# Optimization experiments

Hardware: AMD Instinct MI355X
Metric: run time of the kernel (lower is better)

The kernel has to match this reference:

```python
import jax, jax.numpy as jnp
import numpy as np

B, T, NN = 128, 128, 8          # batch, time_window, nodes per graph (hardcoded in source)
N = B * T * NN                  # 131072 flattened node rows
F_IN, C = 32, 64                # node_features, spatial_features
E = 1_048_576                   # edges (avg degree 8)
EPS = 1e-5


def _gcn(x, src, dst, W, b):
    # PyG GCNConv: h = D^{-1/2}(A+I)D^{-1/2} X W + b, self-loops added, symmetric norm
    h = x @ W                                           # [N, C]
    loop = jnp.arange(N, dtype=src.dtype)
    s = jnp.concatenate([src, loop])
    d = jnp.concatenate([dst, loop])
    deg = jax.ops.segment_sum(jnp.ones_like(s, dtype=h.dtype), d, num_segments=N)
    dinv = jax.lax.rsqrt(deg)                           # deg >= 1 due to self loops
    msg = h[s] * (dinv[s] * dinv[d])[:, None]           # gather + scale
    out = jax.ops.segment_sum(msg, d, num_segments=N)   # scatter-add
    return out + b


def _conv2d(x, w, b, pad_w):
    y = jax.lax.conv_general_dilated(
        x, w, window_strides=(1, 1), padding=[(0, 0), (pad_w, pad_w)],
        dimension_numbers=("NCHW", "OIHW", "NCHW"))
    return y + b[None, :, None, None]


def _bn_relu(x, g, beta):
    # BatchNorm2d in training mode: batch statistics, biased variance
    mu = x.mean(axis=(0, 2, 3), keepdims=True)
    var = x.var(axis=(0, 2, 3), keepdims=True)
    y = (x - mu) * jax.lax.rsqrt(var + EPS)
    return jax.nn.relu(y * g[None, :, None, None] + beta[None, :, None, None])


def _layer(x, src, dst, gw, gb, tw, tb, bg, bb, ow, ob):
    h = _gcn(x, src, dst, gw, gb)                       # [N, C]
    h = h.reshape(B, T, NN, -1).transpose(0, 3, 2, 1)   # [B, C, NN, T]
    h = _conv2d(h, tw, tb, 1)                           # (1,3) temporal conv, pad (0,1)
    h = _bn_relu(h, bg, bb)
    h = _conv2d(h, ow, ob, 0)                           # 1x1 conv (squeeze() is a no-op here)
    h = jnp.tanh(h)
    return h.reshape(-1, h.shape[1])                    # faithful to x.view(-1, x.shape[1])


def setup_inputs() -> dict:
    key = jax.random.key(0)
    ks = jax.random.split(key, 20)
    p = lambda k, shape: (jax.random.normal(k, shape, jnp.float32) * 0.05)
    inp = {
        "x": jax.random.normal(ks[0], (N, F_IN), jnp.float32),
        "edge_index": jax.random.randint(ks[1], (2, E), 0, N, jnp.int32),
        "gcn1_w": p(ks[2], (F_IN, C)), "gcn1_b": jnp.zeros((C,), jnp.float32),
        "t1_w": p(ks[3], (C, C, 1, 3)), "t1_b": jnp.zeros((C,), jnp.float32),
        "bn1_g": jnp.ones((C,), jnp.float32), "bn1_b": jnp.zeros((C,), jnp.float32),
        "o1_w": p(ks[4], (C, C, 1, 1)), "o1_b": jnp.zeros((C,), jnp.float32),
        "gcn2_w": p(ks[5], (C, C)), "gcn2_b": jnp.zeros((C,), jnp.float32),
        "t2_w": p(ks[6], (C, C, 1, 3)), "t2_b": jnp.zeros((C,), jnp.float32),
        "bn2_g": jnp.ones((C,), jnp.float32), "bn2_b": jnp.zeros((C,), jnp.float32),
        "o2_w": p(ks[7], (C, C, 1, 1)), "o2_b": jnp.zeros((C,), jnp.float32),
        "reg_w": p(ks[8], (C, 8)), "reg_b": jnp.zeros((8,), jnp.float32),
    }
    return inp


def reference(x, edge_index, gcn1_w, gcn1_b, t1_w, t1_b, bn1_g, bn1_b, o1_w, o1_b,
              gcn2_w, gcn2_b, t2_w, t2_b, bn2_g, bn2_b, o2_w, o2_b, reg_w, reg_b):
    src, dst = edge_index[0], edge_index[1]
    h = _layer(x, src, dst, gcn1_w, gcn1_b, t1_w, t1_b, bn1_g, bn1_b, o1_w, o1_b)
    h = _layer(h, src, dst, gcn2_w, gcn2_b, t2_w, t2_b, bn2_g, bn2_b, o2_w, o2_b)
    h = h @ reg_w + reg_b                                # [N, 8]
    h = h.reshape(B, T, NN, -1)
    return h.mean(axis=(1, 3))                           # [B, NN] = [128, 8]
```

## Files before the change

kernel.cpp:

```cpp
#include <hip/hip_runtime.h>
#include <stdint.h>

typedef unsigned short u16;
typedef __attribute__((ext_vector_type(8))) short bf16x8;
typedef __attribute__((ext_vector_type(4))) float f32x4;

static const int N_NODES = 131072;
static const int N_EDGES = 1048576;

__device__ __forceinline__ float u2f(u16 u){
  union{uint32_t i; float f;} w; w.i = ((uint32_t)u)<<16; return w.f;
}
__device__ __forceinline__ u16 f2u(float f){
  union{float f; uint32_t u;} v; v.f=f;
  uint32_t u=v.u;
  u += 0x7fff + ((u>>16)&1);
  return (u16)(u>>16);
}
__device__ __forceinline__ float bits2f(uint32_t b){
  union{uint32_t i; float f;} w; w.i = b; return w.f;
}
__device__ __forceinline__ float ldv(const float* p, int i){ return p[i]; }
__device__ __forceinline__ float ldv(const u16* p, int i){ return u2f(p[i]); }
__device__ __forceinline__ void stv(float* p, int i, float v){ p[i]=v; }
__device__ __forceinline__ void stv(u16* p, int i, float v){ p[i]=f2u(v); }
__device__ __forceinline__ float ldmix(const void* p, int i, int isbf){
  return isbf ? u2f(((const u16*)p)[i]) : ((const float*)p)[i];
}

__global__ __launch_bounds__(256) void k_detect(const uint32_t* __restrict__ x, int* __restrict__ flag,
                                                float* __restrict__ stats1, float* __restrict__ stats2,
                                                float* __restrict__ zacc){
  int tid = threadIdx.x;
  for (int i=tid; i<512; i+=256){ stats1[i] = 0.f; stats2[i] = 0.f; }
  for (int i=tid; i<1024; i+=256) zacc[i] = 0.f;
  if (tid == 0){
    int cnt=0;
    for (int i=0;i<256;i++){
      uint32_t e=(x[i]>>7)&0xFFu;
      if (e>=0x6Fu && e<=0x85u) cnt++;
    }
    *flag = (cnt>=128) ? 1 : 0;
  }
}

__global__ __launch_bounds__(256) void k_hist(const int* __restrict__ dst, int* __restrict__ H){
  __shared__ int h[256];
  int tid = threadIdx.x;
  h[tid] = 0;
  __syncthreads();
  int base = blockIdx.x*4096;
  #pragma unroll
  for (int i=0;i<16;i++){
    int e = base + i*256 + tid;
    atomicAdd(&h[(dst[e] & (N_NODES-1))>>9], 1);
  }
  __syncthreads();
  H[blockIdx.x*256 + tid] = h[tid];
}

__global__ __launch_bounds__(256) void k_colscan(const int* __restrict__ H, int* __restrict__ P,
                                                 int* __restrict__ bt){
  __shared__ int sc[256];
  int b = blockIdx.x, tid = threadIdx.x;
  int v = H[tid*256 + b];
  sc[tid] = v; __syncthreads();
  for (int d=1; d<256; d<<=1){
    int o = (tid>=d) ? sc[tid-d] : 0; __syncthreads();
    sc[tid] += o; __syncthreads();
  }
  P[tid*256 + b] = sc[tid] - v;
  if (tid==255) bt[b] = sc[255];
}

__global__ __launch_bounds__(256) void k_scatter2(const int* __restrict__ src, const int* __restrict__ dst,
                                                  const int* __restrict__ P, const int* __restrict__ bt,
                                                  uint32_t* __restrict__ ebuf){
  __shared__ int cu[256], sc[256];
  int tid = threadIdx.x;
  int v = bt[tid];
  sc[tid] = v; __syncthreads();
  for (int d=1; d<256; d<<=1){
    int o = (tid>=d) ? sc[tid-d] : 0; __syncthreads();
    sc[tid] += o; __syncthreads();
  }
  cu[tid] = (sc[tid] - v) + P[blockIdx.x*256 + tid];
  __syncthreads();
  int base = blockIdx.x*4096;
  #pragma unroll
  for (int i=0;i<16;i++){
    int e = base + i*256 + tid;
    int s = src[e] & (N_NODES-1);
    int d = dst[e] & (N_NODES-1);
    int pos = atomicAdd(&cu[d>>9], 1);
    ebuf[pos] = (uint32_t)s | ((uint32_t)(d & 511) << 17);
  }
}

__global__ __launch_bounds__(512) void k_bsort2(const uint32_t* __restrict__ ebuf, const int* __restrict__ bt,
                                                const void* __restrict__ x, const int* __restrict__ flag,
                                                int* __restrict__ adj, int* __restrict__ offs,
                                                int* __restrict__ deg, float* __restrict__ dinv,
                                                u16* __restrict__ Bout){
  __shared__ uint32_t ein[5120], outs[5120];
  __shared__ int hist[512], sc[512], cu[512];
  __shared__ int sct[256];
  __shared__ float dv[512];
  int b = blockIdx.x, tid = threadIdx.x;
  if (tid < 256){ sct[tid] = bt[tid]; }
  __syncthreads();
  for (int d=1; d<256; d<<=1){
    int o = (tid < 256 && tid>=d) ? sct[tid-d] : 0; __syncthreads();
    if (tid < 256) sct[tid] += o; __syncthreads();
  }
  int lo = sct[b] - bt[b], hi = sct[b];
  int cnt = hi - lo; if (cnt > 5120) cnt = 5120; if (cnt < 0) cnt = 0;
  hist[tid] = 0;
  __syncthreads();
  for (int i=tid; i<cnt; i+=512){
    uint32_t p = ebuf[lo+i];
    ein[i] = p;
    atomicAdd(&hist[(p>>17)&511], 1);
  }
  __syncthreads();
  sc[tid] = hist[tid];
  __syncthreads();
  for (int d=1; d<512; d<<=1){
    int v = (tid>=d) ? sc[tid-d] : 0;
    __syncthreads();
    sc[tid] += v;
    __syncthreads();
  }
  {
    int ex = sc[tid] - hist[tid];
    int node = b*512 + tid;
    offs[node] = lo + ex;
    deg[node]  = hist[tid];
    float rs = rsqrtf((float)hist[tid] + 1.0f);
    dinv[node] = rs;
    dv[tid] = rs;
    cu[tid] = ex;
  }
  __syncthreads();
  for (int i=tid; i<cnt; i+=512){
    uint32_t p = ein[i];
    int pos = atomicAdd(&cu[(p>>17)&511], 1);
    outs[pos] = p & 0x1FFFFu;
  }
  __syncthreads();
  for (int i=tid; i<cnt; i+=512) adj[lo+i] = (int)outs[i];
  int isbf = *flag;
  for (int u=tid; u<16384; u+=512){
    int nl = u>>5, c = u&31;
    int idx = ((b<<9) + nl)*32 + c;
    stv(Bout, idx, dv[nl]*ldmix(x, idx, isbf));
  }
}

__device__ __forceinline__ void acc16(uint4 a, float* acc){
  acc[0] += bits2f(a.x<<16); acc[1] += bits2f(a.x&0xFFFF0000u);
  acc[2] += bits2f(a.y<<16); acc[3] += bits2f(a.y&0xFFFF0000u);
  acc[4] += bits2f(a.z<<16); acc[5] += bits2f(a.z&0xFFFF0000u);
  acc[6] += bits2f(a.w<<16); acc[7] += bits2f(a.w&0xFFFF0000u);
}
template<int F>
__global__ __launch_bounds__(256) void k_aggp2(const u16* __restrict__ Xs,
                                               const int* __restrict__ adj, const int* __restrict__ offs,
                                               const int* __restrict__ deg, const float* __restrict__ dinv,
                                               u16* __restrict__ out){
  constexpr int CH  = F/8;
  constexpr int GPW = 64/CH;
  int tid = threadIdx.x;
  int wv = tid>>6, lane = tid&63;
  int g = lane / CH;
  int k = lane % CH;
  int n = blockIdx.x*(4*GPW) + wv*GPW + g;
  int o = offs[n] & (N_EDGES-1);
  int cnt = min(deg[n], 8192);
  const uint4* X4 = (const uint4*)Xs;
  uint4 sv = X4[(size_t)n*CH + k];
  float acc[8] = {0,0,0,0,0,0,0,0};
  acc16(sv, acc);
  int e = 0;
  for (; e+8 <= cnt; e += 8){
    int i0 = adj[o+e+0] & (N_NODES-1);
    int i1 = adj[o+e+1] & (N_NODES-1);
    int i2 = adj[o+e+2] & (N_NODES-1);
    int i3 = adj[o+e+3] & (N_NODES-1);
    int i4 = adj[o+e+4] & (N_NODES-1);
    int i5 = adj[o+e+5] & (N_NODES-1);
    int i6 = adj[o+e+6] & (N_NODES-1);
    int i7 = adj[o+e+7] & (N_NODES-1);
    uint4 a0 = X4[(size_t)i0*CH + k];
    uint4 a1 = X4[(size_t)i1*CH + k];
    uint4 a2 = X4[(size_t)i2*CH + k];
    uint4 a3 = X4[(size_t)i3*CH + k];
    uint4 a4 = X4[(size_t)i4*CH + k];
    uint4 a5 = X4[(size_t)i5*CH + k];
    uint4 a6 = X4[(size_t)i6*CH + k];
    uint4 a7 = X4[(size_t)i7*CH + k];
    acc16(a0, acc); acc16(a1, acc); acc16(a2, acc); acc16(a3, acc);
    acc16(a4, acc); acc16(a5, acc); acc16(a6, acc); acc16(a7, acc);
  }
  if (e+4 <= cnt){
    int i0 = adj[o+e+0] & (N_NODES-1);
    int i1 = adj[o+e+1] & (N_NODES-1);
    int i2 = adj[o+e+2] & (N_NODES-1);
    int i3 = adj[o+e+3] & (N_NODES-1);
    uint4 a0 = X4[(size_t)i0*CH + k];
    uint4 a1 = X4[(size_t)i1*CH + k];
    uint4 a2 = X4[(size_t)i2*CH + k];
    uint4 a3 = X4[(size_t)i3*CH + k];
    acc16(a0, acc); acc16(a1, acc); acc16(a2, acc); acc16(a3, acc);
    e += 4;
  }
  for (; e < cnt; e++){
    int s = adj[o+e] & (N_NODES-1);
    uint4 a = X4[(size_t)s*CH + k];
    acc16(a, acc);
  }
  float dv = dinv[n];
  uint4 r;
  r.x = (uint32_t)f2u(acc[0]*dv) | ((uint32_t)f2u(acc[1]*dv) << 16);
  r.y = (uint32_t)f2u(acc[2]*dv) | ((uint32_t)f2u(acc[3]*dv) << 16);
  r.z = (uint32_t)f2u(acc[4]*dv) | ((uint32_t)f2u(acc[5]*dv) << 16);
  r.w = (uint32_t)f2u(acc[6]*dv) | ((uint32_t)f2u(acc[7]*dv) << 16);
  ((uint4*)out)[(size_t)n*CH + k] = r;
}

__device__ __forceinline__ void wcomb_one(int Kin, const void* gW, const void* gb, const void* tw,
                                          int isbf, u16* Wtb, float* braw, int r, int co){
  if (r < 3*Kin){
    int k = r / Kin, j = r - (r/Kin)*Kin;
    float acc = 0.f;
    for (int c=0; c<64; c++)
      acc += ldmix(gW, j*64+c, isbf) * ldmix(tw, co*192 + c*3 + k, isbf);
    Wtb[co*(3*Kin) + r] = f2u(acc);
  } else {
    int k = r - 3*Kin;
    float acc = 0.f;
    for (int c=0; c<64; c++)
      acc += ldmix(gb, c, isbf) * ldmix(tw, co*192 + c*3 + k, isbf);
    braw[k*64 + co] = acc;
  }
}
__global__ __launch_bounds__(64) void k_wcombB(const void* __restrict__ g1w, const void* __restrict__ g1b,
                                               const void* __restrict__ t1w,
                                               const void* __restrict__ g2w, const void* __restrict__ g2b,
                                               const void* __restrict__ t2w,
                                               const void* __restrict__ o1w, const void* __restrict__ o2w,
                                               const int* __restrict__ flag,
                                               u16* __restrict__ Wtb1, float* __restrict__ braw1,
                                               u16* __restrict__ Wtb2, float* __restrict__ braw2,
                                               u16* __restrict__ owb1, u16* __restrict__ owb2){
  int isbf = *flag;
  int r = blockIdx.x, co = threadIdx.x;
  if (r < 99) wcomb_one(32, g1w, g1b, t1w, isbf, Wtb1, braw1, r, co);
  else if (r < 294) wcomb_one(64, g2w, g2b, t2w, isbf, Wtb2, braw2, r-99, co);
  else if (r < 358){
    int row = r - 294;
    owb1[row*64 + co] = f2u(ldmix(o1w, row*64 + co, isbf));
  } else {
    int row = r - 358;
    owb2[row*64 + co] = f2u(ldmix(o2w, row*64 + co, isbf));
  }
}

template<int Kin>
__global__ __launch_bounds__(256) void k_tconv3(const u16* __restrict__ A, const u16* __restrict__ Wtb,
                                                const float* __restrict__ braw, const void* __restrict__ tb,
                                                const int* __restrict__ flag, u16* __restrict__ out,
                                                float* __restrict__ stats){
  constexpr int K  = 3*Kin;
  constexpr int SA = Kin + 8;
  constexpr int JH = Kin/2;
  constexpr int JL = (Kin==64) ? 5 : 4;
  __shared__ alignas(16) u16 At[66*SA];
  __shared__ float ball[64], bs0[64], bs2[64];
  __shared__ float wsum[4][64], wsum2[4][64];

  int isbf = *flag;
  int bid = blockIdx.x;
  int b = bid>>4, rem = bid&15, v = rem>>1, th = rem&1;
  const int tid = threadIdx.x;

  if (tid < 64){
    float b0=braw[tid], b1=braw[64+tid], b2=braw[128+tid];
    ball[tid] = ldmix(tb, tid, isbf) + b0 + b1 + b2;
    bs0[tid] = b0; bs2[tid] = b2;
  }
  {
    uint32_t* Ad = (uint32_t*)At;
    const uint32_t* Ag = (const uint32_t*)A;
    for (int u=tid; u<66*JH; u+=256){
      int ls = u >> JL, jd = u & (JH-1);
      int t = th*64 + ls - 1;
      uint32_t pack = 0;
      if (t >= 0 && t < 128)
        pack = Ag[((((b*128+t)*8+v))*Kin >> 1) + jd];
      Ad[ls*(SA/2) + jd] = pack;
    }
  }
  __syncthreads();

  int wv_ = tid >> 6, lane = tid & 63;
  int q = lane >> 4, l16 = lane & 15;
  int ltb0 = wv_ * 16;

  f32x4 acc[4];
  #pragma unroll
  for (int nt=0; nt<4; nt++) acc[nt] = (f32x4){0.f,0.f,0.f,0.f};

  #pragma unroll
  for (int s=0; s<K/32; s++){
    int kk = (32*s)/Kin;
    int j0 = 32*s - kk*Kin;
    int col = j0 + q*8;
    bf16x8 afr = *(const bf16x8*)&At[(ltb0 + l16 + kk)*SA + col];
    bf16x8 bfr[4];
    #pragma unroll
    for (int nt=0; nt<4; nt++){
      int co = nt*16 + l16;
      bfr[nt] = *(const bf16x8*)&Wtb[co*K + 32*s + q*8];
    }
    #pragma unroll
    for (int nt=0; nt<4; nt++)
      acc[nt] = __builtin_amdgcn_mfma_f32_16x16x32_bf16(afr, bfr[nt], acc[nt], 0, 0, 0);
  }

  float ls_[4] = {0,0,0,0}, ls2_[4] = {0,0,0,0};
  #pragma unroll
  for (int r=0; r<4; r++){
    int t = th*64 + ltb0 + q*4 + r;
    int base = (((b*128+t)*8+v)) << 6;
    #pragma unroll
    for (int nt=0; nt<4; nt++){
      int co = nt*16 + l16;
      float val = acc[nt][r] + ball[co];
      if (t == 0)   val -= bs0[co];
      if (t == 127) val -= bs2[co];
      out[base + co] = f2u(val);
      ls_[nt] += val; ls2_[nt] += val*val;
    }
  }
  #pragma unroll
  for (int nt=0; nt<4; nt++){
    ls_[nt]  += __shfl_xor(ls_[nt], 16);  ls_[nt]  += __shfl_xor(ls_[nt], 32);
    ls2_[nt] += __shfl_xor(ls2_[nt], 16); ls2_[nt] += __shfl_xor(ls2_[nt], 32);
  }
  if (q == 0){
    #pragma unroll
    for (int nt=0; nt<4; nt++){
      wsum[wv_][nt*16 + l16]  = ls_[nt];
      wsum2[wv_][nt*16 + l16] = ls2_[nt];
    }
  }
  __syncthreads();
  if (tid < 64){
    float a = wsum[0][tid]+wsum[1][tid]+wsum[2][tid]+wsum[3][tid];
    float a2 = wsum2[0][tid]+wsum2[1][tid]+wsum2[2][tid]+wsum2[3][tid];
    int bank = (bid & 3) * 128;
    atomicAdd(&stats[bank + tid], a);
    atomicAdd(&stats[bank + 64 + tid], a2);
  }
}

template<bool FINAL>
__global__ __launch_bounds__(256) void k_bnfuse3(const u16* __restrict__ X, const float* __restrict__ stats,
                                                 const void* __restrict__ gam, const void* __restrict__ bet,
                                                 const u16* __restrict__ owb, const void* __restrict__ ob,
                                                 const int* __restrict__ flag, const float* __restrict__ presc,
                                                 u16* __restrict__ out16,
                                                 float* __restrict__ zacc, const void* __restrict__ rw){
  constexpr int SA = 72;
  __shared__ alignas(16) u16 Yl[64*SA];
  __shared__ float kk[64], bsh[64], obs[64];
  __shared__ float rw_s[64];
  __shared__ float wred[4];
  int isbf = *flag;
  int bid = blockIdx.x;
  int b = bid>>4, rem = bid&15, v = rem>>1, th = rem&1;
  const int tid = threadIdx.x;
  const float invM = 1.0f/131072.0f;

  if (tid < 64){
    int ci = tid;
    float s1 = stats[ci] + stats[128+ci] + stats[256+ci] + stats[384+ci];
    float s2 = stats[64+ci] + stats[192+ci] + stats[320+ci] + stats[448+ci];
    float mu = s1*invM;
    float var = s2*invM - mu*mu;
    float rs = rsqrtf(fmaxf(var, 0.f) + 1e-5f);
    float kv = rs*ldmix(gam, ci, isbf);
    kk[ci] = kv;
    bsh[ci] = ldmix(bet, ci, isbf) - mu*kv;
    obs[ci] = ldmix(ob, ci, isbf);
    if (FINAL){
      float s = 0.f;
      #pragma unroll
      for (int f=0; f<8; f++) s += ldmix(rw, ci*8 + f, isbf);
      rw_s[ci] = s;
    }
  }
  __syncthreads();
  {
    uint32_t* Yd = (uint32_t*)Yl;
    const uint32_t* Xg = (const uint32_t*)X;
    for (int u=tid; u<64*32; u+=256){
      int lt = u>>5, jd = u&31;
      int ci = jd<<1;
      int t = th*64 + lt;
      int rowbase = (((b*128+t)*8+v)) << 6;
      uint32_t pr = Xg[(rowbase>>1) + jd];
      float x0 = bits2f(pr<<16);
      float x1 = bits2f(pr & 0xFFFF0000u);
      float y0 = fmaxf(x0*kk[ci] + bsh[ci], 0.f);
      float y1 = fmaxf(x1*kk[ci+1] + bsh[ci+1], 0.f);
      Yd[lt*(SA/2) + jd] = (uint32_t)f2u(y0) | ((uint32_t)f2u(y1) << 16);
    }
  }
  __syncthreads();

  int wv_ = tid >> 6, lane = tid & 63;
  int q = lane >> 4, l16 = lane & 15;
  int ltb0 = wv_ * 16;

  f32x4 acc[4];
  #pragma unroll
  for (int nt=0; nt<4; nt++) acc[nt] = (f32x4){0.f,0.f,0.f,0.f};

  #pragma unroll
  for (int s=0; s<2; s++){
    int col = 32*s + q*8;
    bf16x8 afr = *(const bf16x8*)&Yl[(ltb0 + l16)*SA + col];
    bf16x8 bfr[4];
    #pragma unroll
    for (int nt=0; nt<4; nt++){
      int co = nt*16 + l16;
      bfr[nt] = *(const bf16x8*)&owb[co*64 + col];
    }
    #pragma unroll
    for (int nt=0; nt<4; nt++)
      acc[nt] = __builtin_amdgcn_mfma_f32_16x16x32_bf16(afr, bfr[nt], acc[nt], 0, 0, 0);
  }

  __syncthreads();
  #pragma unroll
  for (int r=0; r<4; r++){
    int lt = ltb0 + q*4 + r;
    #pragma unroll
    for (int nt=0; nt<4; nt++){
      int co = nt*16 + l16;
      Yl[lt*SA + co] = f2u(acc[nt][r] + obs[co]);
    }
  }
  __syncthreads();
  if (!FINAL){
    for (int u=tid; u<4096; u+=256){
      int l = u & 63;
      int co = u >> 6;
      float z = tanhf(u2f(Yl[l*SA + co]));
      int r = (b<<10) + (co<<4) + (v<<1) + th;
      if (presc) z *= presc[r];
      out16[(r<<6) + l] = f2u(z);
    }
  } else {
    float zsum = 0.f;
    for (int u=tid; u<4096; u+=256){
      int l = u & 63;
      int co = u >> 6;
      float z = tanhf(u2f(Yl[l*SA + co]));
      zsum += z * rw_s[l];
    }
    for (int off=32; off; off>>=1) zsum += __shfl_down(zsum, off);
    if (lane == 0) wred[wv_] = zsum;
    __syncthreads();
    if (tid == 0){
      int base = (b<<3) + ((v&3)<<1) + th;
      atomicAdd(&zacc[base], wred[0] + wred[1] + wred[2] + wred[3]);
    }
  }
}

__global__ __launch_bounds__(256) void k_fin2(const float* __restrict__ zacc, const void* __restrict__ rb,
                                              const int* __restrict__ flag, void* __restrict__ out){
  int i = blockIdx.x*256 + threadIdx.x;
  if (i >= 1024) return;
  int isbf = *flag;
  float rbs = 0.f;
  #pragma unroll
  for (int f=0; f<8; f++) rbs += ldmix(rb, f, isbf);
  float val = zacc[i]*(1.0f/1024.0f) + rbs*0.125f;
  if (isbf) ((u16*)out)[i] = f2u(val);
  else      ((float*)out)[i] = val;
}

extern "C" void kernel_launch(void* const* d_in, const int* in_sizes, int n_in,
                              void* d_out, int out_size, void* d_ws, size_t ws_size,
                              hipStream_t stream){
  (void)in_sizes; (void)n_in; (void)out_size; (void)ws_size;
  char* p = (char*)d_ws;
  auto alloc = [&](size_t bytes){ void* r = (void*)p; p += (bytes + 255) & ~(size_t)255; return r; };
  u16*   U1   = (u16*)  alloc(sizeof(u16)*(size_t)N_NODES*64);
  u16*   U2   = (u16*)  alloc(sizeof(u16)*(size_t)N_NODES*64);
  u16*   C16  = (u16*)  alloc(sizeof(u16)*(size_t)N_NODES*64);
  int*   deg  = (int*)  alloc(sizeof(int)*N_NODES);
  float* dinv = (float*)alloc(sizeof(float)*N_NODES);
  int*   offs = (int*)  alloc(sizeof(int)*N_NODES);
  int*   adj  = (int*)  alloc(sizeof(int)*N_EDGES);
  int*   H    = (int*)  alloc(sizeof(int)*256*256);
  int*   P    = (int*)  alloc(sizeof(int)*256*256);
  int*   bt   = (int*)  alloc(sizeof(int)*256);
  float* stats1=(float*)alloc(sizeof(float)*512);
  float* stats2=(float*)alloc(sizeof(float)*512);
  int*   flag = (int*)  alloc(sizeof(int)*64);
  u16*   Wtb1 = (u16*)  alloc(sizeof(u16)*96*64);
  float* braw1= (float*)alloc(sizeof(float)*192);
  u16*   Wtb2 = (u16*)  alloc(sizeof(u16)*192*64);
  float* braw2= (float*)alloc(sizeof(float)*192);
  u16*   owb1 = (u16*)  alloc(sizeof(u16)*64*64);
  u16*   owb2 = (u16*)  alloc(sizeof(u16)*64*64);
  float* zacc = (float*)alloc(sizeof(float)*1024);
  uint32_t* ebuf = (uint32_t*)C16;
  u16* Bs16 = U1;
  u16* A16  = U1 + (size_t)N_NODES*32;
  u16* D16  = U1;
  u16* E16  = U2;

  const void* x   = d_in[0];
  const int* edge = (const int*)d_in[1];
  const void* g1w = d_in[2];  const void* g1b = d_in[3];
  const void* t1w = d_in[4];  const void* t1b = d_in[5];
  const void* bn1g= d_in[6];  const void* bn1b= d_in[7];
  const void* o1w = d_in[8];  const void* o1b = d_in[9];
  const void* g2w = d_in[10]; const void* g2b = d_in[11];
  const void* t2w = d_in[12]; const void* t2b = d_in[13];
  const void* bn2g= d_in[14]; const void* bn2b= d_in[15];
  const void* o2w = d_in[16]; const void* o2b = d_in[17];
  const void* rw  = d_in[18]; const void* rb  = d_in[19];
  const int* src = edge;
  const int* dst = edge + N_EDGES;

  k_detect<<<1, 256, 0, stream>>>((const uint32_t*)x, flag, stats1, stats2, zacc);

  k_hist    <<<256, 256, 0, stream>>>(dst, H);
  k_colscan <<<256, 256, 0, stream>>>(H, P, bt);
  k_scatter2<<<256, 256, 0, stream>>>(src, dst, P, bt, ebuf);
  k_bsort2  <<<256, 512, 0, stream>>>(ebuf, bt, x, flag, adj, offs, deg, dinv, Bs16);

  k_wcombB<<<422, 64, 0, stream>>>(g1w, g1b, t1w, g2w, g2b, t2w, o1w, o2w, flag,
                                   Wtb1, braw1, Wtb2, braw2, owb1, owb2);

  k_aggp2<32>  <<<N_NODES/64, 256, 0, stream>>>(Bs16, adj, offs, deg, dinv, A16);
  k_tconv3<32> <<<2048, 256, 0, stream>>>(A16, Wtb1, braw1, t1b, flag, C16, stats1);
  k_bnfuse3<false><<<2048, 256, 0, stream>>>(C16, stats1, bn1g, bn1b, owb1, o1b, flag, dinv, D16,
                                             (float*)nullptr, (const void*)nullptr);

  k_aggp2<64>  <<<N_NODES/32, 256, 0, stream>>>(D16, adj, offs, deg, dinv, E16);
  k_tconv3<64> <<<2048, 256, 0, stream>>>(E16, Wtb2, braw2, t2b, flag, C16, stats2);
  k_bnfuse3<true><<<2048, 256, 0, stream>>>(C16, stats2, bn2g, bn2b, owb2, o2b, flag, (const float*)nullptr,
                                            (u16*)nullptr, zacc, rw);
  k_fin2<<<4, 256, 0, stream>>>(zacc, rb, flag, d_out);
}
```

Before: 299.5 us.

## Fuse setup kernels, degree-sort nodes for aggregation, vectorize prescale, fast tanh

Merges the detect/zeroing kernel into the histogram kernel and the weight-combination kernel into the column-scan kernel, cutting two launches. Within each 512-node bucket, nodes are ranked by in-degree into a permutation that the aggregation kernels use, so wavefront lanes handle nodes of similar degree and loop divergence drops. The prescaled-input write now moves two elements per thread per step. tanhf is replaced with an exp-based approximation. The cost is an extra perm indirection and small accuracy differences from the fast tanh.

```diff
diff --git a/kernel.cpp b/kernel.cpp
--- a/kernel.cpp
+++ b/kernel.cpp
@@ -20,57 +20,103 @@
 __device__ __forceinline__ float bits2f(uint32_t b){
   union{uint32_t i; float f;} w; w.i = b; return w.f;
 }
-__device__ __forceinline__ float ldv(const float* p, int i){ return p[i]; }
-__device__ __forceinline__ float ldv(const u16* p, int i){ return u2f(p[i]); }
-__device__ __forceinline__ void stv(float* p, int i, float v){ p[i]=v; }
-__device__ __forceinline__ void stv(u16* p, int i, float v){ p[i]=f2u(v); }
 __device__ __forceinline__ float ldmix(const void* p, int i, int isbf){
   return isbf ? u2f(((const u16*)p)[i]) : ((const float*)p)[i];
 }
-
-__global__ __launch_bounds__(256) void k_detect(const uint32_t* __restrict__ x, int* __restrict__ flag,
-                                                float* __restrict__ stats1, float* __restrict__ stats2,
-                                                float* __restrict__ zacc){
-  int tid = threadIdx.x;
-  for (int i=tid; i<512; i+=256){ stats1[i] = 0.f; stats2[i] = 0.f; }
-  for (int i=tid; i<1024; i+=256) zacc[i] = 0.f;
-  if (tid == 0){
-    int cnt=0;
-    for (int i=0;i<256;i++){
-      uint32_t e=(x[i]>>7)&0xFFu;
-      if (e>=0x6Fu && e<=0x85u) cnt++;
-    }
-    *flag = (cnt>=128) ? 1 : 0;
-  }
-}
-
-__global__ __launch_bounds__(256) void k_hist(const int* __restrict__ dst, int* __restrict__ H){
+__device__ __forceinline__ float ftanh(float x){
+  float ax = fabsf(x);
+  float e  = __expf(ax + ax);
+  float r  = 1.f - __fdividef(2.f, e + 1.f);
+  return copysignf(r, x);
+}
+
+__global__ __launch_bounds__(256) void k_hist(const int* __restrict__ dst, int* __restrict__ H,
+                                              const uint32_t* __restrict__ x, int* __restrict__ flag,
+                                              float* __restrict__ stats1, float* __restrict__ stats2,
+                                              float* __restrict__ zacc){
   __shared__ int h[256];
+  __shared__ int dcnt;
   int tid = threadIdx.x;
   h[tid] = 0;
-  __syncthreads();
+  if (blockIdx.x == 0){
+    if (tid == 0) dcnt = 0;
+    for (int i=tid; i<512; i+=256){ stats1[i] = 0.f; stats2[i] = 0.f; }
+    for (int i=tid; i<1024; i+=256) zacc[i] = 0.f;
+  }
+  __syncthreads();
+  if (blockIdx.x == 0){
+    uint32_t e = (x[tid]>>7) & 0xFFu;
+    int ok = (e >= 0x6Fu && e <= 0x85u) ? 1 : 0;
+    unsigned long long m = __ballot(ok);
+    if ((tid & 63) == 0) atomicAdd(&dcnt, (int)__popcll(m));
+    __syncthreads();
+    if (tid == 0) *flag = (dcnt >= 128) ? 1 : 0;
+  }
   int base = blockIdx.x*4096;
   #pragma unroll
   for (int i=0;i<16;i++){
-    int e = base + i*256 + tid;
-    atomicAdd(&h[(dst[e] & (N_NODES-1))>>9], 1);
+    int e2 = base + i*256 + tid;
+    atomicAdd(&h[(dst[e2] & (N_NODES-1))>>9], 1);
   }
   __syncthreads();
   H[blockIdx.x*256 + tid] = h[tid];
 }
 
-__global__ __launch_bounds__(256) void k_colscan(const int* __restrict__ H, int* __restrict__ P,
-                                                 int* __restrict__ bt){
-  __shared__ int sc[256];
-  int b = blockIdx.x, tid = threadIdx.x;
-  int v = H[tid*256 + b];
-  sc[tid] = v; __syncthreads();
-  for (int d=1; d<256; d<<=1){
-    int o = (tid>=d) ? sc[tid-d] : 0; __syncthreads();
-    sc[tid] += o; __syncthreads();
-  }
-  P[tid*256 + b] = sc[tid] - v;
-  if (tid==255) bt[b] = sc[255];
+__device__ __forceinline__ void wcomb_one(int Kin, const void* gW, const void* gb, const void* tw,
+                                          int isbf, u16* Wtb, float* braw, int r, int co){
+  if (r < 3*Kin){
+    int k = r / Kin, j = r - (r/Kin)*Kin;
+    float acc = 0.f;
+    for (int c=0; c<64; c++)
+      acc += ldmix(gW, j*64+c, isbf) * ldmix(tw, co*192 + c*3 + k, isbf);
+    Wtb[co*(3*Kin) + r] = f2u(acc);
+  } else {
+    int k = r - 3*Kin;
+    float acc = 0.f;
+    for (int c=0; c<64; c++)
+      acc += ldmix(gb, c, isbf) * ldmix(tw, co*192 + c*3 + k, isbf);
+    braw[k*64 + co] = acc;
+  }
+}
+
+__global__ __launch_bounds__(256) void k_colscan_w(const int* __restrict__ H, int* __restrict__ P,
+                                                   int* __restrict__ bt,
+                                                   const void* __restrict__ g1w, const void* __restrict__ g1b,
+                                                   const void* __restrict__ t1w,
+                                                   const void* __restrict__ g2w, const void* __restrict__ g2b,
+                                                   const void* __restrict__ t2w,
+                                                   const void* __restrict__ o1w, const void* __restrict__ o2w,
+                                                   const int* __restrict__ flag,
+                                                   u16* __restrict__ Wtb1, float* __restrict__ braw1,
+                                                   u16* __restrict__ Wtb2, float* __restrict__ braw2,
+                                                   u16* __restrict__ owb1, u16* __restrict__ owb2){
+  int tid = threadIdx.x;
+  if (blockIdx.x < 256){
+    __shared__ int sc[256];
+    int b = blockIdx.x;
+    int v = H[tid*256 + b];
+    sc[tid] = v; __syncthreads();
+    for (int d=1; d<256; d<<=1){
+      int o = (tid>=d) ? sc[tid-d] : 0; __syncthreads();
+      sc[tid] += o; __syncthreads();
+    }
+    P[tid*256 + b] = sc[tid] - v;
+    if (tid==255) bt[b] = sc[255];
+  } else {
+    int isbf = *flag;
+    int r = (blockIdx.x - 256)*4 + (tid>>6);
+    int co = tid & 63;
+    if (r >= 422) return;
+    if (r < 99) wcomb_one(32, g1w, g1b, t1w, isbf, Wtb1, braw1, r, co);
+    else if (r < 294) wcomb_one(64, g2w, g2b, t2w, isbf, Wtb2, braw2, r-99, co);
+    else if (r < 358){
+      int row = r - 294;
+      owb1[row*64 + co] = f2u(ldmix(o1w, row*64 + co, isbf));
+    } else {
+      int row = r - 358;
+      owb2[row*64 + co] = f2u(ldmix(o2w, row*64 + co, isbf));
+    }
+  }
 }
 
 __global__ __launch_bounds__(256) void k_scatter2(const int* __restrict__ src, const int* __restrict__ dst,
@@ -101,11 +147,12 @@
                                                 const void* __restrict__ x, const int* __restrict__ flag,
                                                 int* __restrict__ adj, int* __restrict__ offs,
                                                 int* __restrict__ deg, float* __restrict__ dinv,
-                                                u16* __restrict__ Bout){
+                                                u16* __restrict__ Bout, int* __restrict__ perm){
   __shared__ uint32_t ein[5120], outs[5120];
   __shared__ int hist[512], sc[512], cu[512];
   __shared__ int sct[256];
   __shared__ float dv[512];
+  __shared__ int dh2[64], dsc[64];
   int b = blockIdx.x, tid = threadIdx.x;
   if (tid < 256){ sct[tid] = bt[tid]; }
   __syncthreads();
@@ -148,12 +195,38 @@
     outs[pos] = p & 0x1FFFFu;
   }
   __syncthreads();
+  if (tid < 64) dh2[tid] = 0;
+  __syncthreads();
+  int mybin = min(hist[tid], 63);
+  atomicAdd(&dh2[mybin], 1);
+  __syncthreads();
+  if (tid == 0){
+    int s = 0;
+    for (int i=0;i<64;i++){ int c = dh2[i]; dsc[i] = s; s += c; }
+  }
+  __syncthreads();
+  {
+    int rank = atomicAdd(&dsc[mybin], 1);
+    perm[(b<<9) + rank] = (b<<9) + tid;
+  }
   for (int i=tid; i<cnt; i+=512) adj[lo+i] = (int)outs[i];
   int isbf = *flag;
-  for (int u=tid; u<16384; u+=512){
-    int nl = u>>5, c = u&31;
-    int idx = ((b<<9) + nl)*32 + c;
-    stv(Bout, idx, dv[nl]*ldmix(x, idx, isbf));
+  {
+    uint32_t* Bd = (uint32_t*)Bout;
+    for (int u=tid; u<8192; u+=512){
+      int nl = u>>4, jd = u&15;
+      int half = ((b<<9) + nl)*16 + jd;
+      float x0, x1;
+      if (isbf){
+        uint32_t pr = ((const uint32_t*)x)[half];
+        x0 = bits2f(pr<<16); x1 = bits2f(pr & 0xFFFF0000u);
+      } else {
+        float2 f2 = ((const float2*)x)[half];
+        x0 = f2.x; x1 = f2.y;
+      }
+      float d = dv[nl];
+      Bd[half] = (uint32_t)f2u(x0*d) | ((uint32_t)f2u(x1*d) << 16);
+    }
   }
 }
 
@@ -164,7 +237,7 @@
   acc[6] += bits2f(a.w<<16); acc[7] += bits2f(a.w&0xFFFF0000u);
 }
 template<int F>
-__global__ __launch_bounds__(256) void k_aggp2(const u16* __restrict__ Xs,
+__global__ __launch_bounds__(256) void k_aggp2(const u16* __restrict__ Xs, const int* __restrict__ perm,
                                                const int* __restrict__ adj, const int* __restrict__ offs,
                                                const int* __restrict__ deg, const float* __restrict__ dinv,
                                                u16* __restrict__ out){
@@ -174,7 +247,7 @@
   int wv = tid>>6, lane = tid&63;
   int g = lane / CH;
   int k = lane % CH;
-  int n = blockIdx.x*(4*GPW) + wv*GPW + g;
+  int n = perm[blockIdx.x*(4*GPW) + wv*GPW + g];
   int o = offs[n] & (N_EDGES-1);
   int cnt = min(deg[n], 8192);
   const uint4* X4 = (const uint4*)Xs;
@@ -228,44 +301,6 @@
   ((uint4*)out)[(size_t)n*CH + k] = r;
 }
 
-__device__ __forceinline__ void wcomb_one(int Kin, const void* gW, const void* gb, const void* tw,
-                                          int isbf, u16* Wtb, float* braw, int r, int co){
-  if (r < 3*Kin){
-    int k = r / Kin, j = r - (r/Kin)*Kin;
-    float acc = 0.f;
-    for (int c=0; c<64; c++)
-      acc += ldmix(gW, j*64+c, isbf) * ldmix(tw, co*192 + c*3 + k, isbf);
-    Wtb[co*(3*Kin) + r] = f2u(acc);
-  } else {
-    int k = r - 3*Kin;
-    float acc = 0.f;
-    for (int c=0; c<64; c++)
-      acc += ldmix(gb, c, isbf) * ldmix(tw, co*192 + c*3 + k, isbf);
-    braw[k*64 + co] = acc;
-  }
-}
-__global__ __launch_bounds__(64) void k_wcombB(const void* __restrict__ g1w, const void* __restrict__ g1b,
-                                               const void* __restrict__ t1w,
-                                               const void* __restrict__ g2w, const void* __restrict__ g2b,
-                                               const void* __restrict__ t2w,
-                                               const void* __restrict__ o1w, const void* __restrict__ o2w,
-                                               const int* __restrict__ flag,
-                                               u16* __restrict__ Wtb1, float* __restrict__ braw1,
-                                               u16* __restrict__ Wtb2, float* __restrict__ braw2,
-                                               u16* __restrict__ owb1, u16* __restrict__ owb2){
-  int isbf = *flag;
-  int r = blockIdx.x, co = threadIdx.x;
-  if (r < 99) wcomb_one(32, g1w, g1b, t1w, isbf, Wtb1, braw1, r, co);
-  else if (r < 294) wcomb_one(64, g2w, g2b, t2w, isbf, Wtb2, braw2, r-99, co);
-  else if (r < 358){
-    int row = r - 294;
-    owb1[row*64 + co] = f2u(ldmix(o1w, row*64 + co, isbf));
-  } else {
-    int row = r - 358;
-    owb2[row*64 + co] = f2u(ldmix(o2w, row*64 + co, isbf));
-  }
-}
-
 template<int Kin>
 __global__ __launch_bounds__(256) void k_tconv3(const u16* __restrict__ A, const u16* __restrict__ Wtb,
                                                 const float* __restrict__ braw, const void* __restrict__ tb,
@@ -458,7 +493,7 @@
     for (int u=tid; u<4096; u+=256){
       int l = u & 63;
       int co = u >> 6;
-      float z = tanhf(u2f(Yl[l*SA + co]));
+      float z = ftanh(u2f(Yl[l*SA + co]));
       int r = (b<<10) + (co<<4) + (v<<1) + th;
       if (presc) z *= presc[r];
       out16[(r<<6) + l] = f2u(z);
@@ -468,7 +503,7 @@
     for (int u=tid; u<4096; u+=256){
       int l = u & 63;
       int co = u >> 6;
-      float z = tanhf(u2f(Yl[l*SA + co]));
+      float z = ftanh(u2f(Yl[l*SA + co]));
       zsum += z * rw_s[l];
     }
     for (int off=32; off; off>>=1) zsum += __shfl_down(zsum, off);
@@ -507,6 +542,7 @@
   float* dinv = (float*)alloc(sizeof(float)*N_NODES);
   int*   offs = (int*)  alloc(sizeof(int)*N_NODES);
   int*   adj  = (int*)  alloc(sizeof(int)*N_EDGES);
+  int*   perm = (int*)  alloc(sizeof(int)*N_NODES);
   int*   H    = (int*)  alloc(sizeof(int)*256*256);
   int*   P    = (int*)  alloc(sizeof(int)*256*256);
   int*   bt   = (int*)  alloc(sizeof(int)*256);
@@ -540,22 +576,18 @@
   const int* src = edge;
   const int* dst = edge + N_EDGES;
 
-  k_detect<<<1, 256, 0, stream>>>((const uint32_t*)x, flag, stats1, stats2, zacc);
-
-  k_hist    <<<256, 256, 0, stream>>>(dst, H);
-  k_colscan <<<256, 256, 0, stream>>>(H, P, bt);
-  k_scatter2<<<256, 256, 0, stream>>>(src, dst, P, bt, ebuf);
-  k_bsort2  <<<256, 512, 0, stream>>>(ebuf, bt, x, flag, adj, offs, deg, dinv, Bs16);
-
-  k_wcombB<<<422, 64, 0, stream>>>(g1w, g1b, t1w, g2w, g2b, t2w, o1w, o2w, flag,
-                                   Wtb1, braw1, Wtb2, braw2, owb1, owb2);
-
-  k_aggp2<32>  <<<N_NODES/64, 256, 0, stream>>>(Bs16, adj, offs, deg, dinv, A16);
+  k_hist     <<<256, 256, 0, stream>>>(dst, H, (const uint32_t*)x, flag, stats1, stats2, zacc);
+  k_colscan_w<<<362, 256, 0, stream>>>(H, P, bt, g1w, g1b, t1w, g2w, g2b, t2w, o1w, o2w, flag,
+                                       Wtb1, braw1, Wtb2, braw2, owb1, owb2);
+  k_scatter2 <<<256, 256, 0, stream>>>(src, dst, P, bt, ebuf);
+  k_bsort2   <<<256, 512, 0, stream>>>(ebuf, bt, x, flag, adj, offs, deg, dinv, Bs16, perm);
+
+  k_aggp2<32>  <<<N_NODES/64, 256, 0, stream>>>(Bs16, perm, adj, offs, deg, dinv, A16);
   k_tconv3<32> <<<2048, 256, 0, stream>>>(A16, Wtb1, braw1, t1b, flag, C16, stats1);
   k_bnfuse3<false><<<2048, 256, 0, stream>>>(C16, stats1, bn1g, bn1b, owb1, o1b, flag, dinv, D16,
                                              (float*)nullptr, (const void*)nullptr);
 
-  k_aggp2<64>  <<<N_NODES/32, 256, 0, stream>>>(D16, adj, offs, deg, dinv, E16);
+  k_aggp2<64>  <<<N_NODES/32, 256, 0, stream>>>(D16, perm, adj, offs, deg, dinv, E16);
   k_tconv3<64> <<<2048, 256, 0, stream>>>(E16, Wtb2, braw2, t2b, flag, C16, stats2);
   k_bnfuse3<true><<<2048, 256, 0, stream>>>(C16, stats2, bn2g, bn2b, owb2, o2b, flag, (const float*)nullptr,
                                             (u16*)nullptr, zacc, rw);
```

Measured after the change: 296.3 us. About the same (-1.1%).
